# Kernel optimization log

Hardware: AMD Instinct MI355X
Metric: run time of the kernel (lower is better)

The kernel has to match this reference:

```python
import jax, jax.numpy as jnp
import numpy as np

T_MAX = 16           # max target instance label (labels 1..T_MAX, 0 = background)
CCL_ITERS = 128      # fixed label-propagation iterations for connected components
S1 = 0.7310585786300049    # sigmoid(1.0)
SP0 = 0.6931471805599453   # softplus(0.0) = log 2
SP1 = 1.3132616875182228   # softplus(1.0)


def bce_dice(logits, target):
    # BCEDiceLoss: BCE-with-logits (mean) + soft dice on sigmoid probs
    p = jax.nn.sigmoid(logits)
    bce = jnp.mean(jax.nn.softplus(logits) - logits * target)
    inter = jnp.sum(p * target)
    dice = 1.0 - (2.0 * inter + 1.0) / (jnp.sum(p) + jnp.sum(target) + 1.0)
    return bce + dice


def connected_components(mask):
    # 4-connected components via iterative max-label propagation.
    # mask: [B,H,W] bool. Returns int32 label map; component id = max flat index in component + 1.
    B, H, W = mask.shape
    init = jnp.where(mask, jnp.arange(1, B * H * W + 1, dtype=jnp.int32).reshape(B, H, W), 0)

    def step(lab, _):
        up = jnp.pad(lab, ((0, 0), (1, 0), (0, 0)))[:, :H, :]
        dn = jnp.pad(lab, ((0, 0), (0, 1), (0, 0)))[:, 1:, :]
        lf = jnp.pad(lab, ((0, 0), (0, 0), (1, 0)))[:, :, :W]
        rt = jnp.pad(lab, ((0, 0), (0, 0), (0, 1)))[:, :, 1:]
        nb = jnp.maximum(jnp.maximum(up, dn), jnp.maximum(lf, rt))
        return jnp.where(mask, jnp.maximum(lab, nb), 0), None

    lab, _ = jax.lax.scan(step, init, None, length=CCL_ITERS)
    return lab


def _forward(pred_out, target_mask):
    B, C, H, W = pred_out.shape
    N = B * H * W
    Nf = jnp.float32(N)

    pm = jnp.argmax(pred_out, axis=1)          # [B,H,W] in {0,1} since C=2
    fg = pm > 0                                 # predicted foreground

    # base loss on channel-1 logits masked to predicted foreground vs binarized target
    res = bce_dice(pred_out[:, 1:2] * fg[:, None].astype(pred_out.dtype),
                   (target_mask > 0).astype(jnp.float32))

    # relabel predicted foreground into connected components (global unique ids)
    lab = connected_components(fg)              # [B,H,W]
    comp = jnp.where(fg, lab - 1, 0).reshape(-1)          # component root id in [0,N)
    tgt = target_mask[:, 0].reshape(-1).astype(jnp.int32)  # target label 0..T_MAX
    w = fg.reshape(-1).astype(jnp.float32)

    # confusion counts: inter[p, t] = |{pixels: pred comp p AND target label t}|
    inter = jax.ops.segment_sum(w, comp * (T_MAX + 1) + tgt,
                                num_segments=N * (T_MAX + 1)).reshape(N, T_MAX + 1)
    cnt_p = inter.sum(axis=1)                                       # [N] pred comp sizes
    cnt_t = jax.ops.segment_sum(jnp.ones((N,), jnp.float32), tgt,
                                num_segments=T_MAX + 1)             # [T+1] target sizes

    def pair_losses(inter_t, ct):
        # BCEDice between binary comp mask (as logits in {0,1}) and binary target mask,
        # expressed in closed form from the confusion counts.
        bce = (Nf * SP0 + cnt_p * (SP1 - SP0) - inter_t) / Nf
        sum_pt = 0.5 * ct + (S1 - 0.5) * inter_t
        sum_p = 0.5 * Nf + (S1 - 0.5) * cnt_p
        dice = 1.0 - (2.0 * sum_pt + 1.0) / (sum_p + ct + 1.0)
        return bce + dice

    def step(carry, t):
        used, acc, matched, un_tgt = carry
        ct = cnt_t[t]
        present = ct > 0
        avail = (cnt_p > 0) & (~used)
        any_avail = jnp.any(avail)
        losses = jnp.where(avail, pair_losses(inter[:, t], ct), jnp.inf)
        idx = jnp.argmin(losses)
        do = present & any_avail
        acc = acc + jnp.where(do, losses[idx], 0.0)
        used = used.at[idx].set(used[idx] | do)
        matched = matched + do.astype(jnp.float32)
        un_tgt = un_tgt + (present & (~any_avail)).astype(jnp.float32)
        return (used, acc, matched, un_tgt), None

    carry0 = (jnp.zeros((N,), bool), res, jnp.float32(0.0), jnp.float32(0.0))
    (used, acc, matched, un_tgt), _ = jax.lax.scan(step, carry0, jnp.arange(1, T_MAX + 1))

    n_pred = jnp.sum((cnt_p > 0).astype(jnp.float32))   # total pred components
    return acc + (n_pred - matched) + un_tgt            # penalties for unmatched comps/targets


def setup_inputs() -> dict:
    key = jax.random.key(0)
    k1, k2 = jax.random.split(key)
    pred_out = jax.random.normal(k1, (4, 2, 512, 512), dtype=jnp.float32)
    target_mask = jax.random.randint(k2, (4, 1, 512, 512), 0, 17, dtype=jnp.int32)
    return {"pred_out": pred_out, "target_mask": target_mask}


def reference(pred_out, target_mask):
    return _forward(pred_out, target_mask)
```

## Files before the change

### kernel.cpp

```cpp
#include <hip/hip_runtime.h>
#include <math.h>

#define HH 512
#define WW 512
#define HWSZ (HH * WW)
#define NB 4
#define NPIX (NB * HWSZ)
#define TMAX 16

#define CAP 131072
#define NPART 24
#define NBLK 1024
#define SBLK 512

struct Scalars {
  double sums[4];
  int cnt_t[TMAX + 1];
  int n_comp;
};

__device__ __forceinline__ float pair_loss(float cp, float it, float ctf) {
  const float Nf = (float)NPIX;
  float bce = (Nf * 0.69314718f + cp * 0.62011451f - it) / Nf;
  float sum_pt = 0.5f * ctf + 0.23105858f * it;
  float sum_p = 0.5f * Nf + 0.23105858f * cp;
  float dice = 1.0f - (2.0f * sum_pt + 1.0f) / (sum_p + ctf + 1.0f);
  return bce + dice;
}

__device__ __forceinline__ int chaseRO(const int* __restrict__ P, int x) {
  int p = P[x];
  while (p != x) { x = p; p = P[x]; }
  return x;
}
__device__ __forceinline__ int findRootH(int* P, int x) {
  int p = P[x];
  while (p != x) {
    int gp = P[p];
    if (gp == p) return p;
    P[x] = gp;
    x = gp; p = P[x];
  }
  return x;
}
__device__ void unite(int* P, int a, int b) {
  a = findRootH(P, a);
  b = findRootH(P, b);
  for (;;) {
    if (a == b) return;
    if (a > b) { int t = a; a = b; b = t; }
    int old = atomicMax(&P[a], b);
    if (old == a) return;
    a = findRootH(P, old);
    b = findRootH(P, b);
  }
}

__global__ __launch_bounds__(256) void k_init(const float* __restrict__ pred,
                                              const int* __restrict__ tgt,
                                              int* __restrict__ P,
                                              int* __restrict__ cnt,
                                              double* __restrict__ part) {
  __shared__ int hist[TMAX + 1];
  __shared__ double red[4][4];
  int tid = threadIdx.x;
  if (tid <= TMAX) hist[tid] = 0;
  __syncthreads();
  int g = blockIdx.x * 256 + tid;
  int i = g << 2;
  int b = i >> 18;
  int hw = i & (HWSZ - 1);
  const float* pb = pred + ((size_t)(b << 1)) * HWSZ;
  float4 p0 = *(const float4*)(pb + hw);
  float4 p1 = *(const float4*)(pb + HWSZ + hw);
  int4 tv = *(const int4*)(tgt + i);
  int4 lv;
  float s0 = 0.f, s1 = 0.f, s2 = 0.f, s3 = 0.f;
#define ELEM(P0, P1, TV, IDX, LOUT)                              \
  {                                                              \
    bool fg = (P1) > (P0);                                       \
    float logit = fg ? (P1) : 0.0f;                              \
    float tb = ((TV) > 0) ? 1.0f : 0.0f;                         \
    float sp = fmaxf(logit, 0.0f) + log1pf(expf(-fabsf(logit))); \
    s0 += sp - logit * tb;                                       \
    float pr = 1.0f / (1.0f + expf(-logit));                     \
    s1 += pr; s2 += pr * tb; s3 += tb;                           \
    atomicAdd(&hist[TV], 1);                                     \
    LOUT = fg ? (IDX) : -1;                                      \
  }
  ELEM(p0.x, p1.x, tv.x, i + 0, lv.x)
  ELEM(p0.y, p1.y, tv.y, i + 1, lv.y)
  ELEM(p0.z, p1.z, tv.z, i + 2, lv.z)
  ELEM(p0.w, p1.w, tv.w, i + 3, lv.w)
#undef ELEM
  *(int4*)(P + i) = lv;
  *(int4*)(cnt + i) = make_int4(0, 0, 0, 0);
  for (int o = 32; o > 0; o >>= 1) {
    s0 += __shfl_down(s0, o);
    s1 += __shfl_down(s1, o);
    s2 += __shfl_down(s2, o);
    s3 += __shfl_down(s3, o);
  }
  int lane = tid & 63, wid = tid >> 6;
  if (!lane) { red[wid][0] = s0; red[wid][1] = s1; red[wid][2] = s2; red[wid][3] = s3; }
  __syncthreads();
  double* row = part + (size_t)blockIdx.x * NPART;
  if (tid <= TMAX) row[4 + tid] = (double)hist[tid];
  if (!tid) {
    row[0] = red[0][0] + red[1][0] + red[2][0] + red[3][0];
    row[1] = red[0][1] + red[1][1] + red[2][1] + red[3][1];
    row[2] = red[0][2] + red[1][2] + red[2][2] + red[3][2];
    row[3] = red[0][3] + red[1][3] + red[2][3] + red[3][3];
  }
}

__global__ __launch_bounds__(256) void k_linkred(int* __restrict__ P,
                                                 const double* __restrict__ part,
                                                 Scalars* __restrict__ sc) {
  int tid = threadIdx.x;
  int bid = blockIdx.x;
  int lane = tid & 63, wv = tid >> 6;
  if (bid == 0) {
    double v[21];
#pragma unroll
    for (int j = 0; j < 21; ++j) v[j] = 0.0;
    for (int r = tid; r < NBLK; r += 256) {
      const double* row = part + (size_t)r * NPART;
#pragma unroll
      for (int j = 0; j < 21; ++j) v[j] += row[j];
    }
#pragma unroll
    for (int o = 32; o > 0; o >>= 1) {
#pragma unroll
      for (int j = 0; j < 21; ++j) v[j] += __shfl_down(v[j], o);
    }
    __shared__ double redr[4][21];
    if (!lane) {
#pragma unroll
      for (int j = 0; j < 21; ++j) redr[wv][j] = v[j];
    }
    __syncthreads();
    if (!tid) {
#pragma unroll
      for (int j = 0; j < 21; ++j) v[j] = redr[0][j] + redr[1][j] + redr[2][j] + redr[3][j];
      sc->sums[0] = v[0]; sc->sums[1] = v[1]; sc->sums[2] = v[2]; sc->sums[3] = v[3];
      for (int j = 0; j <= TMAX; ++j) sc->cnt_t[j] = (int)(v[4 + j] + 0.5);
    }
  }
  int base = bid << 10;
#pragma unroll
  for (int k = 0; k < 4; ++k) {
    int i = base + (k << 8) + tid;
    if (P[i] >= 0) {
      int hw = i & (HWSZ - 1);
      int h = hw >> 9;
      int w = hw & (WW - 1);
      if (w < WW - 1 && P[i + 1] >= 0)  unite(P, i, i + 1);
      if (h < HH - 1 && P[i + WW] >= 0) unite(P, i, i + WW);
    }
  }
}

__global__ __launch_bounds__(256) void k_flat(int* __restrict__ P,
                                              int* __restrict__ cnt,
                                              int* __restrict__ interD) {
  int g = blockIdx.x * 256 + threadIdx.x;
  *(int4*)(interD + ((size_t)g << 3)) = make_int4(0, 0, 0, 0);
  *(int4*)(interD + ((size_t)g << 3) + 4) = make_int4(0, 0, 0, 0);
  int i0 = g << 2;
  int4 pv = *(const int4*)(P + i0);
  int4 rv;
  rv.x = (pv.x < 0) ? -1 : chaseRO(P, pv.x);
  rv.y = (pv.y < 0) ? -1 : chaseRO(P, pv.y);
  rv.z = (pv.z < 0) ? -1 : chaseRO(P, pv.z);
  rv.w = (pv.w < 0) ? -1 : chaseRO(P, pv.w);
  *(int4*)(P + i0) = rv;
  if (rv.x >= 0) atomicAdd(&cnt[rv.x], 1);
  if (rv.y >= 0) atomicAdd(&cnt[rv.y], 1);
  if (rv.z >= 0) atomicAdd(&cnt[rv.z], 1);
  if (rv.w >= 0) atomicAdd(&cnt[rv.w], 1);
}

__global__ __launch_bounds__(256) void k_bcnt(const int* __restrict__ cnt,
                                              int* __restrict__ bcnt) {
  __shared__ int redi[4];
  int tid = threadIdx.x;
  int base = blockIdx.x << 10;
  int4 cv = *(const int4*)(cnt + base + (tid << 2));
  int c = (cv.x > 0) + (cv.y > 0) + (cv.z > 0) + (cv.w > 0);
  for (int o = 32; o > 0; o >>= 1) c += __shfl_down(c, o);
  int lane = tid & 63, wv = tid >> 6;
  if (!lane) redi[wv] = c;
  __syncthreads();
  if (!tid) bcnt[blockIdx.x] = redi[0] + redi[1] + redi[2] + redi[3];
}

__global__ __launch_bounds__(256) void k_scatter(int* __restrict__ cnt,
                                                 const int* __restrict__ bcnt,
                                                 int* __restrict__ cntD,
                                                 Scalars* __restrict__ sc) {
  __shared__ int redi[4];
  __shared__ int redp4[4];
  __shared__ int wtot[4];
  int tid = threadIdx.x;
  int bid = blockIdx.x;
  int lane = tid & 63, wv = tid >> 6;
  int base = bid << 10;
  int4 cv = *(const int4*)(cnt + base + (tid << 2));
  int val[4] = { cv.x, cv.y, cv.z, cv.w };
  int cme = (cv.x > 0) + (cv.y > 0) + (cv.z > 0) + (cv.w > 0);
  int4 bv = *(const int4*)(bcnt + (tid << 2));
  int j0 = tid << 2;
  int tot = bv.x + bv.y + bv.z + bv.w;
  int pre = ((j0 + 0 < bid) ? bv.x : 0) + ((j0 + 1 < bid) ? bv.y : 0)
          + ((j0 + 2 < bid) ? bv.z : 0) + ((j0 + 3 < bid) ? bv.w : 0);
  for (int o = 32; o > 0; o >>= 1) {
    tot += __shfl_down(tot, o);
    pre += __shfl_down(pre, o);
  }
  if (!lane) { redi[wv] = tot; redp4[wv] = pre; }
  __syncthreads();
  tot = redi[0] + redi[1] + redi[2] + redi[3];
  pre = redp4[0] + redp4[1] + redp4[2] + redp4[3];
  if (bid == 0 && tid == 0) sc->n_comp = tot;
  int v = cme;
  for (int o = 1; o < 64; o <<= 1) {
    int u = __shfl_up(v, o);
    if (lane >= o) v += u;
  }
  if (lane == 63) wtot[wv] = v;
  __syncthreads();
  int add = 0;
  for (int w = 0; w < wv; ++w) add += wtot[w];
  int d = pre + v + add - cme;
#pragma unroll
  for (int k = 0; k < 4; ++k) {
    int c = val[k];
    if (c > 0) {
      if (d < CAP) cntD[d] = c;
      cnt[base + (tid << 2) + k] = d;
      ++d;
    }
  }
}

__global__ __launch_bounds__(256) void k_interall(const int* __restrict__ P,
                                                  const int* __restrict__ tgt,
                                                  const int* __restrict__ dense_of,
                                                  int* __restrict__ interD) {
  int g = blockIdx.x * 256 + threadIdx.x;
  int i0 = g << 2;
  int4 rv = *(const int4*)(P + i0);
  int4 tv = *(const int4*)(tgt + i0);
#define DO(R, T)                                                     \
  if ((R) >= 0 && (T)) {                                             \
    int dd = dense_of[R];                                            \
    if ((unsigned)dd < CAP) atomicAdd(&interD[((size_t)dd << 4) + (T) - 1], 1); \
  }
  DO(rv.x, tv.x) DO(rv.y, tv.y) DO(rv.z, tv.z) DO(rv.w, tv.w)
#undef DO
}

__global__ __launch_bounds__(256) void k_scanmins(const Scalars* __restrict__ sc,
                                                  const int* __restrict__ cntD,
                                                  const int* __restrict__ interD,
                                                  unsigned long long* __restrict__ bm) {
  int tid = threadIdx.x;
  int d = blockIdx.x * 256 + tid;
  int n_comp = sc->n_comp;
  int c = (d < n_comp) ? cntD[d] : 0;
  int itv[16];
  if (c > 0) {
#pragma unroll
    for (int k = 0; k < 4; ++k) {
      int4 r = *(const int4*)(interD + ((size_t)d << 4) + (k << 2));
      itv[(k << 2) + 0] = r.x; itv[(k << 2) + 1] = r.y;
      itv[(k << 2) + 2] = r.z; itv[(k << 2) + 3] = r.w;
    }
  }
  __shared__ unsigned long long wmin[4][16];
  float cp = (float)c;
  int lane = tid & 63, wv = tid >> 6;
#pragma unroll
  for (int t = 0; t < 16; ++t) {
    unsigned long long key = ~0ULL;
    if (c > 0) {
      float loss = pair_loss(cp, (float)itv[t], (float)sc->cnt_t[t + 1]);
      key = ((unsigned long long)__float_as_uint(loss) << 32) | (unsigned)d;
    }
    for (int o = 32; o > 0; o >>= 1) {
      unsigned long long kk = __shfl_down(key, o);
      if (kk < key) key = kk;
    }
    if (!lane) wmin[wv][t] = key;
  }
  __syncthreads();
  if (tid < 16) {
    unsigned long long m = wmin[0][tid];
    if (wmin[1][tid] < m) m = wmin[1][tid];
    if (wmin[2][tid] < m) m = wmin[2][tid];
    if (wmin[3][tid] < m) m = wmin[3][tid];
    bm[(size_t)tid * SBLK + blockIdx.x] = m;
  }
}

__global__ __launch_bounds__(256) void k_greedy(const Scalars* __restrict__ sc,
                                                const int* __restrict__ cntD,
                                                const int* __restrict__ interD,
                                                unsigned long long* __restrict__ bm,
                                                float* __restrict__ out) {
  __shared__ int s_used[16];
  __shared__ int s_nused;
  __shared__ unsigned long long s_m;
  __shared__ int s_state;
  __shared__ unsigned long long wmin[4];
  int tid = threadIdx.x;
  int lane = tid & 63, wv = tid >> 6;
  if (!tid) s_nused = 0;
  __syncthreads();
  double acc = 0.0;
  int matched = 0, un = 0;
  int n_comp = sc->n_comp;
  for (int t = 1; t <= TMAX; ++t) {
    int ct = sc->cnt_t[t];
    if (ct == 0) continue;
    for (int iter = 0; iter < 64; ++iter) {
      const unsigned long long* row = bm + (size_t)(t - 1) * SBLK;
      unsigned long long k1 = row[tid];
      unsigned long long k2 = row[tid + 256];
      unsigned long long key = (k2 < k1) ? k2 : k1;
      for (int o = 32; o > 0; o >>= 1) {
        unsigned long long kk = __shfl_down(key, o);
        if (kk < key) key = kk;
      }
      if (!lane) wmin[wv] = key;
      __syncthreads();
      if (!tid) {
        unsigned long long m = wmin[0];
        if (wmin[1] < m) m = wmin[1];
        if (wmin[2] < m) m = wmin[2];
        if (wmin[3] < m) m = wmin[3];
        s_m = m;
        int st = 0;
        if (m == ~0ULL) st = 2;
        else {
          int dd = (int)(m & 0xFFFFFFFFu);
          for (int u = 0; u < s_nused; ++u)
            if (s_used[u] == dd) { st = 1; break; }
        }
        s_state = st;
      }
      __syncthreads();
      int st = s_state;
      unsigned long long m = s_m;
      if (st == 0) {
        acc += (double)__uint_as_float((unsigned)(m >> 32));
        matched += 1;
        if (!tid) { s_used[s_nused] = (int)(m & 0xFFFFFFFFu); s_nused++; }
        break;
      } else if (st == 2) {
        un += 1;
        break;
      } else {
        int dd = (int)(m & 0xFFFFFFFFu);
        int b = dd >> 8;
        int d2 = (b << 8) + tid;
        unsigned long long nk = ~0ULL;
        int c = (d2 < n_comp) ? cntD[d2] : 0;
        if (c > 0) {
          bool ex = false;
          for (int u = 0; u < s_nused; ++u)
            if (s_used[u] == d2) { ex = true; break; }
          if (!ex) {
            float loss = pair_loss((float)c, (float)interD[((size_t)d2 << 4) + (t - 1)], (float)ct);
            nk = ((unsigned long long)__float_as_uint(loss) << 32) | (unsigned)d2;
          }
        }
        for (int o = 32; o > 0; o >>= 1) {
          unsigned long long kk = __shfl_down(nk, o);
          if (kk < nk) nk = kk;
        }
        if (!lane) wmin[wv] = nk;
        __syncthreads();
        if (!tid) {
          unsigned long long mm = wmin[0];
          if (wmin[1] < mm) mm = wmin[1];
          if (wmin[2] < mm) mm = wmin[2];
          if (wmin[3] < mm) mm = wmin[3];
          bm[(size_t)(t - 1) * SBLK + b] = mm;
        }
        __syncthreads();
      }
    }
    __syncthreads();
  }
  if (!tid) {
    double Nd = (double)NPIX;
    double res = sc->sums[0] / Nd
               + 1.0 - (2.0 * sc->sums[2] + 1.0) / (sc->sums[1] + sc->sums[3] + 1.0);
    out[0] = (float)(res + acc + (double)(n_comp - matched) + (double)un);
  }
}

extern "C" void kernel_launch(void* const* d_in, const int* in_sizes, int n_in,
                              void* d_out, int out_size, void* d_ws, size_t ws_size,
                              hipStream_t stream) {
  (void)in_sizes; (void)n_in; (void)out_size; (void)ws_size;
  const float* pred = (const float*)d_in[0];
  const int* tgt = (const int*)d_in[1];
  float* out = (float*)d_out;

  char* w = (char*)d_ws;
  int* P     = (int*)w;            w += (size_t)NPIX * 4;
  int* cnt   = (int*)w;            w += (size_t)NPIX * 4;
  double* part = (double*)w;       w += (size_t)NBLK * NPART * 8;
  Scalars* sc = (Scalars*)w;       w += 256;
  int* bcnt  = (int*)w;            w += 4096;
  int* cntD  = (int*)w;            w += (size_t)CAP * 4;
  unsigned long long* bm = (unsigned long long*)w; w += (size_t)16 * SBLK * 8;
  int* interD = (int*)w;

  k_init<<<NBLK, 256, 0, stream>>>(pred, tgt, P, cnt, part);
  k_linkred<<<NBLK, 256, 0, stream>>>(P, part, sc);
  k_flat<<<NBLK, 256, 0, stream>>>(P, cnt, interD);
  k_bcnt<<<NBLK, 256, 0, stream>>>(cnt, bcnt);
  k_scatter<<<NBLK, 256, 0, stream>>>(cnt, bcnt, cntD, sc);
  k_interall<<<NBLK, 256, 0, stream>>>(P, tgt, cnt, interD);
  k_scanmins<<<SBLK, 256, 0, stream>>>(sc, cntD, interD, bm);
  k_greedy<<<1, 256, 0, stream>>>(sc, cntD, interD, bm, out);
}
```

Measured before the change: 145.9 us.

## Two-phase CCL: shared-memory tile union-find, then seam-only global merge

Connected-component labeling is split into two kernels. The first runs union-find inside each 32x32 tile in shared memory, then writes tile-local roots and component sizes to global memory. The second merges only the edges along tile seams with global atomic unions, on a reduced grid. k_flat now moves each tile root's size to its final root instead of issuing one atomic per pixel. This cuts global atomic traffic and pointer chasing. The risk is that the int4 write-back of counts can overwrite atomic adds landing on neighbouring entries in the same vector.

Result: slower. 207.3 us (+42.1%).

```diff
diff --git a/kernel.cpp b/kernel.cpp
--- a/kernel.cpp
+++ b/kernel.cpp
@@ -12,6 +12,12 @@
 #define NPART 24
 #define NBLK 1024
 #define SBLK 512
+
+#define TS 32
+#define SEAMS 15
+#define EDGES_PER_DIR (NB * SEAMS * HH)
+#define NEDGES (2 * EDGES_PER_DIR)
+#define BORDER_BLOCKS 64
 
 struct Scalars {
   double sums[4];
@@ -53,6 +59,23 @@
     if (old == a) return;
     a = findRootH(P, old);
     b = findRootH(P, b);
+  }
+}
+__device__ __forceinline__ int findL(const int* lp, int x) {
+  int p = lp[x];
+  while (p != x) { x = p; p = lp[x]; }
+  return x;
+}
+__device__ void uniteL(int* lp, int a, int b) {
+  a = findL(lp, a);
+  b = findL(lp, b);
+  for (;;) {
+    if (a == b) return;
+    if (a > b) { int t = a; a = b; b = t; }
+    int old = atomicMax(&lp[a], b);
+    if (old == a) return;
+    a = findL(lp, old);
+    b = findL(lp, b);
   }
 }
 
@@ -114,13 +137,70 @@
   }
 }
 
-__global__ __launch_bounds__(256) void k_linkred(int* __restrict__ P,
-                                                 const double* __restrict__ part,
-                                                 Scalars* __restrict__ sc) {
+__global__ __launch_bounds__(256) void k_local(int* __restrict__ P,
+                                               int* __restrict__ cnt) {
+  __shared__ int lp[TS * TS];
+  __shared__ int sz[TS * TS];
   int tid = threadIdx.x;
   int bid = blockIdx.x;
-  int lane = tid & 63, wv = tid >> 6;
+  int b = bid >> 8;
+  int ty = (bid >> 4) & 15, tx = bid & 15;
+  int oh = ty << 5, ow = tx << 5;
+  int gbase = b * HWSZ + (oh << 9) + ow;
+
+  int fgv[4];
+#pragma unroll
+  for (int k = 0; k < 4; ++k) {
+    int c = (k << 8) + tid;
+    int r = c >> 5, q = c & 31;
+    int gi = gbase + (r << 9) + q;
+    fgv[k] = P[gi];
+    lp[c] = (fgv[k] >= 0) ? c : -1;
+    sz[c] = 0;
+  }
+  __syncthreads();
+#pragma unroll
+  for (int k = 0; k < 4; ++k) {
+    int c = (k << 8) + tid;
+    if (lp[c] >= 0) {
+      int r = c >> 5, q = c & 31;
+      if (q < TS - 1 && lp[c + 1] >= 0)  uniteL(lp, c, c + 1);
+      if (r < TS - 1 && lp[c + TS] >= 0) uniteL(lp, c, c + TS);
+    }
+  }
+  __syncthreads();
+  int rootc[4];
+#pragma unroll
+  for (int k = 0; k < 4; ++k) {
+    int c = (k << 8) + tid;
+    if (lp[c] >= 0) {
+      int rr = findL(lp, c);
+      rootc[k] = rr;
+      atomicAdd(&sz[rr], 1);
+    } else rootc[k] = -1;
+  }
+  __syncthreads();
+#pragma unroll
+  for (int k = 0; k < 4; ++k) {
+    int c = (k << 8) + tid;
+    int rr = rootc[k];
+    if (rr >= 0) {
+      int r = c >> 5, q = c & 31;
+      int gi = gbase + (r << 9) + q;
+      int groot = gbase + ((rr >> 5) << 9) + (rr & 31);
+      P[gi] = groot;
+      if (c == rr) cnt[gi] = sz[c];
+    }
+  }
+}
+
+__global__ __launch_bounds__(256) void k_border(int* __restrict__ P,
+                                                const double* __restrict__ part,
+                                                Scalars* __restrict__ sc) {
+  int tid = threadIdx.x;
+  int bid = blockIdx.x;
   if (bid == 0) {
+    int lane = tid & 63, wv = tid >> 6;
     double v[21];
 #pragma unroll
     for (int j = 0; j < 21; ++j) v[j] = 0.0;
@@ -147,17 +227,24 @@
       for (int j = 0; j <= TMAX; ++j) sc->cnt_t[j] = (int)(v[4 + j] + 0.5);
     }
   }
-  int base = bid << 10;
-#pragma unroll
-  for (int k = 0; k < 4; ++k) {
-    int i = base + (k << 8) + tid;
-    if (P[i] >= 0) {
-      int hw = i & (HWSZ - 1);
-      int h = hw >> 9;
-      int w = hw & (WW - 1);
-      if (w < WW - 1 && P[i + 1] >= 0)  unite(P, i, i + 1);
-      if (h < HH - 1 && P[i + WW] >= 0) unite(P, i, i + WW);
-    }
+  for (int e = bid * 256 + tid; e < NEDGES; e += BORDER_BLOCKS * 256) {
+    int dir = e >= EDGES_PER_DIR;
+    int e2 = dir ? e - EDGES_PER_DIR : e;
+    int b = e2 / (SEAMS * HH);
+    int r2 = e2 - b * (SEAMS * HH);
+    int seam = r2 >> 9;
+    int pos = r2 & 511;
+    int i, j;
+    if (!dir) {
+      int w = (TS - 1) + (seam << 5);
+      i = b * HWSZ + (pos << 9) + w;
+      j = i + 1;
+    } else {
+      int h = (TS - 1) + (seam << 5);
+      i = b * HWSZ + (h << 9) + pos;
+      j = i + WW;
+    }
+    if (P[i] >= 0 && P[j] >= 0) unite(P, i, j);
   }
 }
 
@@ -169,16 +256,26 @@
   *(int4*)(interD + ((size_t)g << 3) + 4) = make_int4(0, 0, 0, 0);
   int i0 = g << 2;
   int4 pv = *(const int4*)(P + i0);
+  int4 cv = *(const int4*)(cnt + i0);
   int4 rv;
   rv.x = (pv.x < 0) ? -1 : chaseRO(P, pv.x);
   rv.y = (pv.y < 0) ? -1 : chaseRO(P, pv.y);
   rv.z = (pv.z < 0) ? -1 : chaseRO(P, pv.z);
   rv.w = (pv.w < 0) ? -1 : chaseRO(P, pv.w);
   *(int4*)(P + i0) = rv;
-  if (rv.x >= 0) atomicAdd(&cnt[rv.x], 1);
-  if (rv.y >= 0) atomicAdd(&cnt[rv.y], 1);
-  if (rv.z >= 0) atomicAdd(&cnt[rv.z], 1);
-  if (rv.w >= 0) atomicAdd(&cnt[rv.w], 1);
+  int nz = 0;
+#define MOVE(K, R, C)                                      \
+  if ((C) > 0 && (R) != i0 + (K)) {                        \
+    atomicAdd(&cnt[R], (C));                               \
+    nz = 1; cv_arr[K] = 0;                                 \
+  }
+  int cv_arr[4] = { cv.x, cv.y, cv.z, cv.w };
+  MOVE(0, rv.x, cv_arr[0])
+  MOVE(1, rv.y, cv_arr[1])
+  MOVE(2, rv.z, cv_arr[2])
+  MOVE(3, rv.w, cv_arr[3])
+#undef MOVE
+  if (nz) *(int4*)(cnt + i0) = make_int4(cv_arr[0], cv_arr[1], cv_arr[2], cv_arr[3]);
 }
 
 __global__ __launch_bounds__(256) void k_bcnt(const int* __restrict__ cnt,
@@ -421,7 +518,8 @@
   int* interD = (int*)w;
 
   k_init<<<NBLK, 256, 0, stream>>>(pred, tgt, P, cnt, part);
-  k_linkred<<<NBLK, 256, 0, stream>>>(P, part, sc);
+  k_local<<<NBLK, 256, 0, stream>>>(P, cnt);
+  k_border<<<BORDER_BLOCKS, 256, 0, stream>>>(P, part, sc);
   k_flat<<<NBLK, 256, 0, stream>>>(P, cnt, interD);
   k_bcnt<<<NBLK, 256, 0, stream>>>(cnt, bcnt);
   k_scatter<<<NBLK, 256, 0, stream>>>(cnt, bcnt, cntD, sc);
```
